# Performance work log

Hardware: AMD Instinct MI355X
Metric: run time of the kernel (lower is better)

## Reference

```python
import jax, jax.numpy as jnp
import numpy as np

B = 8192
DIMS = [1024, 1024, 1024, 1024]  # input, hidden0, hidden1, output
RANK = 64


def _apg_layer(x, Wm, bm, U, V, b, activate):
    # hyper-net (MLP_Layer with no hidden units == single Linear): generates rank*rank weights per sample
    w = (x @ Wm.T + bm).reshape(x.shape[0], RANK, RANK)   # [B, r, r]
    u = x @ U.T                                           # U_matrix: [B, r]
    # (u.unsqueeze(-1) * w).sum(-2) == per-sample matvec
    h = jnp.einsum('br,brs->bs', u, w)                    # [B, r]
    out = h @ V.T + b                                     # V_matrix + static bias: [B, out]
    return jax.nn.relu(out) if activate else out


def setup_inputs() -> dict:
    key = jax.random.key(0)
    ks = jax.random.split(key, 16)
    inp = {"x": jax.random.normal(ks[0], (B, DIMS[0]), dtype=jnp.float32)}
    ki = 1
    for l in range(3):
        din, dout = DIMS[l], DIMS[l + 1]
        inp[f"Wm{l}"] = jax.random.normal(ks[ki], (RANK * RANK, din), dtype=jnp.float32) * (1.0 / np.sqrt(din)); ki += 1
        inp[f"bm{l}"] = jnp.zeros((RANK * RANK,), dtype=jnp.float32)
        inp[f"U{l}"] = jax.random.normal(ks[ki], (RANK, din), dtype=jnp.float32) * (1.0 / np.sqrt(din)); ki += 1
        inp[f"V{l}"] = jax.random.normal(ks[ki], (dout, RANK), dtype=jnp.float32) * (1.0 / np.sqrt(RANK)); ki += 1
        inp[f"b{l}"] = jnp.zeros((dout,), dtype=jnp.float32)
    return inp


def reference(x, Wm0, bm0, U0, V0, b0, Wm1, bm1, U1, V1, b1, Wm2, bm2, U2, V2, b2):
    h = _apg_layer(x, Wm0, bm0, U0, V0, b0, activate=True)   # hidden layer 0 + ReLU
    h = _apg_layer(h, Wm1, bm1, U1, V1, b1, activate=True)   # hidden layer 1 + ReLU
    out = _apg_layer(h, Wm2, bm2, U2, V2, b2, activate=False)  # output layer, no activation
    return out
```

## Files before the change

kernel.cpp:

```cpp
#include <hip/hip_runtime.h>
#include <stdint.h>

typedef short bf16x8_t __attribute__((ext_vector_type(8)));
typedef short bf16x4_t __attribute__((ext_vector_type(4)));
typedef float f32x4_t __attribute__((ext_vector_type(4)));
typedef unsigned short u16x4_t __attribute__((ext_vector_type(4)));

#define DEV static __device__ __forceinline__

DEV float bf2f(unsigned short u) {
  union { unsigned int i; float f; } v; v.i = ((unsigned int)u) << 16; return v.f;
}
DEV unsigned short f2bf(float f) {
  union { float f; unsigned int i; } v; v.f = f;
  unsigned int x = v.i;
  unsigned int lsb = (x >> 16) & 1u;
  x += 0x7fffu + lsb;
  return (unsigned short)(x >> 16);
}

struct CvtTab {
  const float* src[10];
  unsigned short* dst[10];
  int bstart[10];
};

__global__ __launch_bounds__(256) void cvt_all_k(CvtTab t) {
  int bi = blockIdx.x;
  int seg = 0;
#pragma unroll
  for (int s = 1; s < 10; s++) seg += (bi >= t.bstart[s]) ? 1 : 0;
  int local = (bi - t.bstart[seg]) * 256 + threadIdx.x;
  const float* src = t.src[seg];
  unsigned short* dst = t.dst[seg];
  float4 v = ((const float4*)src)[local];
  u16x4_t o = { f2bf(v.x), f2bf(v.y), f2bf(v.z), f2bf(v.w) };
  *(u16x4_t*)&dst[local * 4] = o;
}

__global__ __launch_bounds__(256, 2) void u_splitk(
    const unsigned short* __restrict__ A,
    const unsigned short* __restrict__ Ub,
    float* __restrict__ part) {
  __shared__ unsigned short As[128 * 64];
  __shared__ unsigned short Us[64 * 64];

  const int tid = threadIdx.x;
  const int lane = tid & 63;
  const int w = tid >> 6;
  const int rowBase = blockIdx.y * 128;
  const int kBase = blockIdx.x * 256;

  const int rl = lane >> 3;
  const int kbs = lane & 7;
  const int kbg = kbs ^ rl;
  const int fr = lane & 15;
  const int quad = lane >> 4;

  f32x4_t acc[2][4];
#pragma unroll
  for (int i = 0; i < 2; i++)
#pragma unroll
    for (int j = 0; j < 4; j++) acc[i][j] = f32x4_t{0.f, 0.f, 0.f, 0.f};

  for (int kt = kBase; kt < kBase + 256; kt += 64) {
    __syncthreads();
#pragma unroll
    for (int jj = 0; jj < 4; ++jj) {
      int tr = w * 32 + jj * 8 + rl;
      const unsigned short* ga = A + (size_t)(rowBase + tr) * 1024 + kt + kbg * 8;
      __builtin_amdgcn_global_load_lds(
          (const __attribute__((address_space(1))) void*)ga,
          (__attribute__((address_space(3))) void*)&As[(w * 32 + jj * 8) * 64],
          16, 0, 0);
    }
#pragma unroll
    for (int jj = 0; jj < 2; ++jj) {
      int tr = w * 16 + jj * 8 + rl;
      const unsigned short* gu = Ub + (size_t)tr * 1024 + kt + kbg * 8;
      __builtin_amdgcn_global_load_lds(
          (const __attribute__((address_space(1))) void*)gu,
          (__attribute__((address_space(3))) void*)&Us[(w * 16 + jj * 8) * 64],
          16, 0, 0);
    }
    __syncthreads();

#pragma unroll
    for (int ks = 0; ks < 2; ++ks) {
      bf16x8_t a[2], b[4];
#pragma unroll
      for (int i = 0; i < 2; i++) {
        int m = w * 32 + i * 16 + fr;
        int slot = (ks * 4 + quad) ^ (m & 7);
        a[i] = *(const bf16x8_t*)&As[m * 64 + slot * 8];
      }
#pragma unroll
      for (int j = 0; j < 4; j++) {
        int n = j * 16 + fr;
        int slot = (ks * 4 + quad) ^ (n & 7);
        b[j] = *(const bf16x8_t*)&Us[n * 64 + slot * 8];
      }
#pragma unroll
      for (int i = 0; i < 2; i++)
#pragma unroll
        for (int j = 0; j < 4; j++)
          acc[i][j] = __builtin_amdgcn_mfma_f32_16x16x32_bf16(a[i], b[j],
                                                              acc[i][j], 0, 0, 0);
    }
  }

  float* pp = part + ((size_t)blockIdx.x * 8192 + rowBase) * 64;
#pragma unroll
  for (int i = 0; i < 2; i++)
#pragma unroll
    for (int j = 0; j < 4; j++)
#pragma unroll
      for (int r = 0; r < 4; r++) {
        int row = w * 32 + i * 16 + quad * 4 + r;
        pp[(size_t)row * 64 + j * 16 + fr] = acc[i][j][r];
      }
}

__global__ __launch_bounds__(256) void u_reduce_k(
    const float* __restrict__ part, unsigned short* __restrict__ ug) {
  int i = blockIdx.x * 256 + threadIdx.x;
  float4 s0 = ((const float4*)part)[i];
  float4 s1 = ((const float4*)part)[i + 131072];
  float4 s2 = ((const float4*)part)[i + 262144];
  float4 s3 = ((const float4*)part)[i + 393216];
  u16x4_t o = { f2bf(s0.x + s1.x + s2.x + s3.x),
                f2bf(s0.y + s1.y + s2.y + s3.y),
                f2bf(s0.z + s1.z + s2.z + s3.z),
                f2bf(s0.w + s1.w + s2.w + s3.w) };
  *(u16x4_t*)&ug[i * 4] = o;
}

template <int OUTF32, int RELU, int BIAS>
__global__ __launch_bounds__(256, 2) void gemm_bt(
    const unsigned short* __restrict__ A, const unsigned short* __restrict__ B,
    const float* __restrict__ bias, void* __restrict__ Cout,
    int M, int N, int K) {
  __shared__ unsigned short As[128 * 64];
  __shared__ unsigned short Bs[128 * 64];

  const int tid = threadIdx.x;
  const int lane = tid & 63;
  const int w = tid >> 6;
  const int wrow0 = (w & 1) * 64;
  const int wcol0 = (w >> 1) * 64;
  const int rowBase = blockIdx.y * 128;
  const int colBase = blockIdx.x * 128;

  const int rl = lane >> 3;
  const int kbs = lane & 7;
  const int kbg = kbs ^ rl;
  const int fr = lane & 15;
  const int quad = lane >> 4;

  f32x4_t acc[4][4];
#pragma unroll
  for (int i = 0; i < 4; i++)
#pragma unroll
    for (int j = 0; j < 4; j++) acc[i][j] = f32x4_t{0.f, 0.f, 0.f, 0.f};

  for (int kt = 0; kt < K; kt += 64) {
    __syncthreads();
#pragma unroll
    for (int jj = 0; jj < 4; ++jj) {
      int tr = w * 32 + jj * 8 + rl;
      const unsigned short* ga = A + (size_t)(rowBase + tr) * K + kt + kbg * 8;
      const unsigned short* gb = B + (size_t)(colBase + tr) * K + kt + kbg * 8;
      __builtin_amdgcn_global_load_lds(
          (const __attribute__((address_space(1))) void*)ga,
          (__attribute__((address_space(3))) void*)&As[(w * 32 + jj * 8) * 64],
          16, 0, 0);
      __builtin_amdgcn_global_load_lds(
          (const __attribute__((address_space(1))) void*)gb,
          (__attribute__((address_space(3))) void*)&Bs[(w * 32 + jj * 8) * 64],
          16, 0, 0);
    }
    __syncthreads();

#pragma unroll
    for (int ks = 0; ks < 2; ++ks) {
      bf16x8_t a[4], b[4];
#pragma unroll
      for (int i = 0; i < 4; i++) {
        int m = wrow0 + i * 16 + fr;
        int slot = (ks * 4 + quad) ^ (m & 7);
        a[i] = *(const bf16x8_t*)&As[m * 64 + slot * 8];
      }
#pragma unroll
      for (int j = 0; j < 4; j++) {
        int n = wcol0 + j * 16 + fr;
        int slot = (ks * 4 + quad) ^ (n & 7);
        b[j] = *(const bf16x8_t*)&Bs[n * 64 + slot * 8];
      }
#pragma unroll
      for (int i = 0; i < 4; i++)
#pragma unroll
        for (int j = 0; j < 4; j++)
          acc[i][j] = __builtin_amdgcn_mfma_f32_16x16x32_bf16(a[i], b[j],
                                                              acc[i][j], 0, 0, 0);
    }
  }

#pragma unroll
  for (int j = 0; j < 4; j++) {
    int col = colBase + wcol0 + j * 16 + fr;
    float bv = BIAS ? bias[col] : 0.0f;
#pragma unroll
    for (int i = 0; i < 4; i++) {
#pragma unroll
      for (int r = 0; r < 4; r++) {
        int row = rowBase + wrow0 + i * 16 + quad * 4 + r;
        float v = acc[i][j][r] + bv;
        if (RELU) v = v > 0.f ? v : 0.f;
        if (OUTF32)
          ((float*)Cout)[(size_t)row * N + col] = v;
        else
          ((unsigned short*)Cout)[(size_t)row * N + col] = f2bf(v);
      }
    }
  }
}

__global__ __launch_bounds__(256, 2) void gemm_fused(
    const unsigned short* __restrict__ A,
    const unsigned short* __restrict__ Wmb,
    const unsigned short* __restrict__ ug,
    const float* __restrict__ bm,
    unsigned short* __restrict__ h_out) {
  __shared__ unsigned short smem[16384];
  unsigned short* As = smem;
  unsigned short* Bs = smem + 8192;
  const int K = 1024;

  const int tid = threadIdx.x;
  const int lane = tid & 63;
  const int w = tid >> 6;
  const int wrow0 = (w & 1) * 64;
  const int wcol0 = (w >> 1) * 64;
  const int rowBase = blockIdx.y * 128;
  const int colBase = blockIdx.x * 128;

  const int rl = lane >> 3;
  const int kbs = lane & 7;
  const int kbg = kbs ^ rl;
  const int fr = lane & 15;
  const int quad = lane >> 4;

  f32x4_t acc[4][4];
#pragma unroll
  for (int i = 0; i < 4; i++)
#pragma unroll
    for (int j = 0; j < 4; j++) acc[i][j] = f32x4_t{0.f, 0.f, 0.f, 0.f};

  for (int kt = 0; kt < K; kt += 64) {
    __syncthreads();
#pragma unroll
    for (int jj = 0; jj < 4; ++jj) {
      int tr = w * 32 + jj * 8 + rl;
      int ct = colBase + tr;
      int pr = ((ct & 63) << 6) | (ct >> 6);
      const unsigned short* ga = A + (size_t)(rowBase + tr) * K + kt + kbg * 8;
      const unsigned short* gb = Wmb + (size_t)pr * K + kt + kbg * 8;
      __builtin_amdgcn_global_load_lds(
          (const __attribute__((address_space(1))) void*)ga,
          (__attribute__((address_space(3))) void*)&As[(w * 32 + jj * 8) * 64],
          16, 0, 0);
      __builtin_amdgcn_global_load_lds(
          (const __attribute__((address_space(1))) void*)gb,
          (__attribute__((address_space(3))) void*)&Bs[(w * 32 + jj * 8) * 64],
          16, 0, 0);
    }
    __syncthreads();

#pragma unroll
    for (int ks = 0; ks < 2; ++ks) {
      bf16x8_t a[4], b[4];
#pragma unroll
      for (int i = 0; i < 4; i++) {
        int m = wrow0 + i * 16 + fr;
        int slot = (ks * 4 + quad) ^ (m & 7);
        a[i] = *(const bf16x8_t*)&As[m * 64 + slot * 8];
      }
#pragma unroll
      for (int j = 0; j < 4; j++) {
        int n = wcol0 + j * 16 + fr;
        int slot = (ks * 4 + quad) ^ (n & 7);
        b[j] = *(const bf16x8_t*)&Bs[n * 64 + slot * 8];
      }
#pragma unroll
      for (int i = 0; i < 4; i++)
#pragma unroll
        for (int j = 0; j < 4; j++)
          acc[i][j] = __builtin_amdgcn_mfma_f32_16x16x32_bf16(a[i], b[j],
                                                              acc[i][j], 0, 0, 0);
    }
  }

  __syncthreads();

  {
    int row = tid >> 1;
    int c0 = (tid & 1) * 32;
    const unsigned short* up = ug + (size_t)(rowBase + row) * 64 + c0;
    bf16x8_t v0 = *(const bf16x8_t*)(up);
    bf16x8_t v1 = *(const bf16x8_t*)(up + 8);
    bf16x8_t v2 = *(const bf16x8_t*)(up + 16);
    bf16x8_t v3 = *(const bf16x8_t*)(up + 24);
#pragma unroll
    for (int m = 0; m < 8; m++) {
      smem[(c0 + m) * 136 + row] = (unsigned short)v0[m];
      smem[(c0 + 8 + m) * 136 + row] = (unsigned short)v1[m];
      smem[(c0 + 16 + m) * 136 + row] = (unsigned short)v2[m];
      smem[(c0 + 24 + m) * 136 + row] = (unsigned short)v3[m];
    }
  }
  __syncthreads();

  const int s = blockIdx.x * 2 + (w >> 1);
  float bmv[4];
#pragma unroll
  for (int j = 0; j < 4; j++) bmv[j] = bm[(j * 16 + fr) * 64 + s];

#pragma unroll
  for (int i = 0; i < 4; i++) {
    int row0 = wrow0 + i * 16 + quad * 4;
    bf16x4_t uv[4];
#pragma unroll
    for (int j = 0; j < 4; j++)
      uv[j] = *(const bf16x4_t*)&smem[(j * 16 + fr) * 136 + row0];
#pragma unroll
    for (int r = 0; r < 4; r++) {
      float p = 0.f;
#pragma unroll
      for (int j = 0; j < 4; j++)
        p += bf2f((unsigned short)uv[j][r]) * (acc[i][j][r] + bmv[j]);
      p += __shfl_xor(p, 1, 64);
      p += __shfl_xor(p, 2, 64);
      p += __shfl_xor(p, 4, 64);
      p += __shfl_xor(p, 8, 64);
      if (fr == 0)
        h_out[(size_t)(rowBase + row0 + r) * 64 + s] = f2bf(p);
    }
  }
}

__global__ __launch_bounds__(256, 2) void vu_fused(
    const unsigned short* __restrict__ h,
    const unsigned short* __restrict__ Vb,
    const float* __restrict__ bias,
    const unsigned short* __restrict__ Un,
    unsigned short* __restrict__ act,
    unsigned short* __restrict__ u_out) {
  __shared__ unsigned short tlds[4 * 16 * 72];
  __shared__ float upart[4 * 16 * 68];

  const int tid = threadIdx.x;
  const int lane = tid & 63;
  const int w = tid >> 6;
  const int fr = lane & 15;
  const int quad = lane >> 4;
  const int rowBase = blockIdx.x * 16;

  unsigned short* tl = &tlds[w * 16 * 72];

  bf16x8_t ah0 = *(const bf16x8_t*)&h[(size_t)(rowBase + fr) * 64 + quad * 8];
  bf16x8_t ah1 = *(const bf16x8_t*)&h[(size_t)(rowBase + fr) * 64 + 32 + quad * 8];

  f32x4_t uacc[4];
#pragma unroll
  for (int n = 0; n < 4; n++) uacc[n] = f32x4_t{0.f, 0.f, 0.f, 0.f};

  for (int it = 0; it < 4; ++it) {
    const int cb = w * 256 + it * 64;

    f32x4_t tacc[4];
#pragma unroll
    for (int nt = 0; nt < 4; nt++) {
      const unsigned short* vrow = Vb + (size_t)(cb + nt * 16 + fr) * 64;
      bf16x8_t b0 = *(const bf16x8_t*)&vrow[quad * 8];
      bf16x8_t b1 = *(const bf16x8_t*)&vrow[32 + quad * 8];
      f32x4_t z = {0.f, 0.f, 0.f, 0.f};
      z = __builtin_amdgcn_mfma_f32_16x16x32_bf16(ah0, b0, z, 0, 0, 0);
      tacc[nt] = __builtin_amdgcn_mfma_f32_16x16x32_bf16(ah1, b1, z, 0, 0, 0);
    }

#pragma unroll
    for (int nt = 0; nt < 4; nt++) {
      float bv = bias[cb + nt * 16 + fr];
#pragma unroll
      for (int r = 0; r < 4; r++) {
        float v = tacc[nt][r] + bv;
        v = v > 0.f ? v : 0.f;
        tl[(quad * 4 + r) * 72 + nt * 16 + fr] = f2bf(v);
      }
    }

    {
      int m2 = lane >> 2;
      int kc = (lane & 3) * 16;
      bf16x8_t t0 = *(const bf16x8_t*)&tl[m2 * 72 + kc];
      bf16x8_t t1 = *(const bf16x8_t*)&tl[m2 * 72 + kc + 8];
      unsigned short* ap = act + (size_t)(rowBase + m2) * 1024 + cb + kc;
      *(bf16x8_t*)ap = t0;
      *(bf16x8_t*)(ap + 8) = t1;
    }

#pragma unroll
    for (int ks = 0; ks < 2; ++ks) {
      bf16x8_t at = *(const bf16x8_t*)&tl[fr * 72 + ks * 32 + quad * 8];
#pragma unroll
      for (int n = 0; n < 4; n++) {
        bf16x8_t bu = *(const bf16x8_t*)&Un[(size_t)(n * 16 + fr) * 1024 + cb +
                                            ks * 32 + quad * 8];
        uacc[n] = __builtin_amdgcn_mfma_f32_16x16x32_bf16(at, bu, uacc[n], 0, 0, 0);
      }
    }
  }

  {
    float* up = &upart[w * 16 * 68];
#pragma unroll
    for (int n = 0; n < 4; n++)
#pragma unroll
      for (int r = 0; r < 4; r++)
        up[(quad * 4 + r) * 68 + n * 16 + fr] = uacc[n][r];
  }
  __syncthreads();
  {
    int m = tid >> 4;
    int c0 = (tid & 15) * 4;
    f32x4_t s = {0.f, 0.f, 0.f, 0.f};
#pragma unroll
    for (int wv = 0; wv < 4; wv++)
      s += *(const f32x4_t*)&upart[wv * 16 * 68 + m * 68 + c0];
    u16x4_t o = { f2bf(s[0]), f2bf(s[1]), f2bf(s[2]), f2bf(s[3]) };
    *(u16x4_t*)&u_out[(size_t)(rowBase + m) * 64 + c0] = o;
  }
}

extern "C" void kernel_launch(void* const* d_in, const int* in_sizes, int n_in,
                              void* d_out, int out_size, void* d_ws,
                              size_t ws_size, hipStream_t stream) {
  const float* x = (const float*)d_in[0];
  const float* Wm[3] = {(const float*)d_in[1], (const float*)d_in[6], (const float*)d_in[11]};
  const float* bm[3] = {(const float*)d_in[2], (const float*)d_in[7], (const float*)d_in[12]};
  const float* U[3]  = {(const float*)d_in[3], (const float*)d_in[8], (const float*)d_in[13]};
  const float* V[3]  = {(const float*)d_in[4], (const float*)d_in[9], (const float*)d_in[14]};
  const float* bs[3] = {(const float*)d_in[5], (const float*)d_in[10], (const float*)d_in[15]};

  char* p = (char*)d_ws;
  unsigned short* xb = (unsigned short*)p;  p += 8192UL * 1024 * 2;
  unsigned short* act = (unsigned short*)p; p += 8192UL * 1024 * 2;
  unsigned short* Wmb[3];
  for (int l = 0; l < 3; l++) { Wmb[l] = (unsigned short*)p; p += 4096UL * 1024 * 2; }
  unsigned short* Ub[3];
  for (int l = 0; l < 3; l++) { Ub[l] = (unsigned short*)p; p += 64UL * 1024 * 2; }
  unsigned short* Vb[3];
  for (int l = 0; l < 3; l++) { Vb[l] = (unsigned short*)p; p += 1024UL * 64 * 2; }
  unsigned short* hb = (unsigned short*)p;  p += 8192UL * 64 * 2;
  unsigned short* ug = (unsigned short*)p;  p += 8192UL * 64 * 2;
  float* ug_part = (float*)p;               p += 4UL * 8192 * 64 * 4;

  CvtTab t;
  t.src[0] = x;  t.dst[0] = xb;
  for (int l = 0; l < 3; l++) { t.src[1 + l] = Wm[l]; t.dst[1 + l] = Wmb[l]; }
  for (int l = 0; l < 3; l++) { t.src[4 + l] = U[l];  t.dst[4 + l] = Ub[l]; }
  for (int l = 0; l < 3; l++) { t.src[7 + l] = V[l];  t.dst[7 + l] = Vb[l]; }
  int bs_tab[10] = {8192, 4096, 4096, 4096, 64, 64, 64, 64, 64, 64};
  int acc_b = 0;
  for (int s = 0; s < 10; s++) { t.bstart[s] = acc_b; acc_b += bs_tab[s]; }
  cvt_all_k<<<acc_b, 256, 0, stream>>>(t);

  u_splitk<<<dim3(4, 64), 256, 0, stream>>>(xb, Ub[0], ug_part);
  u_reduce_k<<<512, 256, 0, stream>>>(ug_part, ug);

  const unsigned short* cur = xb;
  for (int l = 0; l < 3; l++) {
    gemm_fused<<<dim3(32, 64), 256, 0, stream>>>(cur, Wmb[l], ug, bm[l], hb);
    if (l < 2) {
      vu_fused<<<512, 256, 0, stream>>>(hb, Vb[l], bs[l], Ub[l + 1], act, ug);
      cur = act;
    } else {
      gemm_bt<1, 0, 1><<<dim3(8, 64), 256, 0, stream>>>(
          hb, Vb[2], bs[2], d_out, 8192, 1024, 64);
    }
  }
}
```

Measured before the change: 420.9 us.

## Merge all phases into one persistent cooperative kernel with grid syncs

Replaces the chain of separate launches (convert, U split-K, reduce, three hyper-GEMMs, VU fused, final GEMM) with a single cooperative persistent kernel. Phases are separated by grid-wide syncs, and hyper-GEMM tiles are handed out through atomic counters. The U0 split-K now uses 8 slices of 128 instead of 4 of 256. This removes launch gaps and tail effects between kernels, at the cost of grid-sync overhead, a fixed grid size and possibly lower occupancy for the persistent blocks. A fallback path keeps the multi-kernel launches.

```diff
diff --git a/kernel.cpp b/kernel.cpp
--- a/kernel.cpp
+++ b/kernel.cpp
@@ -1,5 +1,8 @@
 #include <hip/hip_runtime.h>
+#include <hip/hip_cooperative_groups.h>
 #include <stdint.h>
+
+namespace cg = cooperative_groups;
 
 typedef short bf16x8_t __attribute__((ext_vector_type(8)));
 typedef short bf16x4_t __attribute__((ext_vector_type(4)));
@@ -19,41 +22,50 @@
   return (unsigned short)(x >> 16);
 }
 
-struct CvtTab {
-  const float* src[10];
-  unsigned short* dst[10];
-  int bstart[10];
+struct MegaArgs {
+  const float* fsrc[10];
+  unsigned short* fdst[10];
+  const float* bm[3];
+  const float* bb[3];
+  unsigned short* xb;
+  unsigned short* act;
+  unsigned short* Wmb[3];
+  unsigned short* Ub[3];
+  unsigned short* Vb[3];
+  unsigned short* hb;
+  unsigned short* ug;
+  float* ug_part;
+  float* out;
+  int* counters;
 };
 
-__global__ __launch_bounds__(256) void cvt_all_k(CvtTab t) {
-  int bi = blockIdx.x;
-  int seg = 0;
-#pragma unroll
-  for (int s = 1; s < 10; s++) seg += (bi >= t.bstart[s]) ? 1 : 0;
-  int local = (bi - t.bstart[seg]) * 256 + threadIdx.x;
-  const float* src = t.src[seg];
-  unsigned short* dst = t.dst[seg];
-  float4 v = ((const float4*)src)[local];
-  u16x4_t o = { f2bf(v.x), f2bf(v.y), f2bf(v.z), f2bf(v.w) };
-  *(u16x4_t*)&dst[local * 4] = o;
-}
-
-__global__ __launch_bounds__(256, 2) void u_splitk(
-    const unsigned short* __restrict__ A,
-    const unsigned short* __restrict__ Ub,
-    float* __restrict__ part) {
-  __shared__ unsigned short As[128 * 64];
-  __shared__ unsigned short Us[64 * 64];
-
-  const int tid = threadIdx.x;
+DEV void phase_cvt(const MegaArgs& A, int bid, int tid, int NB) {
+  const int bstart[11] = {0, 8192, 12288, 16384, 20480, 20544, 20608,
+                          20672, 20736, 20800, 20864};
+  for (int vb = bid; vb < 20864; vb += NB) {
+    int seg = 0;
+#pragma unroll
+    for (int s = 1; s < 10; s++) seg += (vb >= bstart[s]) ? 1 : 0;
+    int local = (vb - bstart[seg]) * 256 + tid;
+    float4 v = ((const float4*)A.fsrc[seg])[local];
+    u16x4_t o = { f2bf(v.x), f2bf(v.y), f2bf(v.z), f2bf(v.w) };
+    *(u16x4_t*)&A.fdst[seg][local * 4] = o;
+  }
+}
+
+DEV void u0_splitk_vb(const unsigned short* __restrict__ Acur,
+                      const unsigned short* __restrict__ Ub,
+                      float* __restrict__ part,
+                      unsigned short* smem, int vb, int tid) {
+  unsigned short* As = smem;
+  unsigned short* Us = smem + 8192;
   const int lane = tid & 63;
   const int w = tid >> 6;
-  const int rowBase = blockIdx.y * 128;
-  const int kBase = blockIdx.x * 256;
-
+  const int ks = vb >> 6;
+  const int rowBase = (vb & 63) * 128;
+  const int kBase = ks * 128;
   const int rl = lane >> 3;
-  const int kbs = lane & 7;
-  const int kbg = kbs ^ rl;
+  const int kbg = (lane & 7) ^ rl;
   const int fr = lane & 15;
   const int quad = lane >> 4;
 
@@ -63,12 +75,12 @@
 #pragma unroll
     for (int j = 0; j < 4; j++) acc[i][j] = f32x4_t{0.f, 0.f, 0.f, 0.f};
 
-  for (int kt = kBase; kt < kBase + 256; kt += 64) {
+  for (int kt = kBase; kt < kBase + 128; kt += 64) {
     __syncthreads();
 #pragma unroll
     for (int jj = 0; jj < 4; ++jj) {
       int tr = w * 32 + jj * 8 + rl;
-      const unsigned short* ga = A + (size_t)(rowBase + tr) * 1024 + kt + kbg * 8;
+      const unsigned short* ga = Acur + (size_t)(rowBase + tr) * 1024 + kt + kbg * 8;
       __builtin_amdgcn_global_load_lds(
           (const __attribute__((address_space(1))) void*)ga,
           (__attribute__((address_space(3))) void*)&As[(w * 32 + jj * 8) * 64],
@@ -86,18 +98,18 @@
     __syncthreads();
 
 #pragma unroll
-    for (int ks = 0; ks < 2; ++ks) {
+    for (int ksi = 0; ksi < 2; ++ksi) {
       bf16x8_t a[2], b[4];
 #pragma unroll
       for (int i = 0; i < 2; i++) {
         int m = w * 32 + i * 16 + fr;
-        int slot = (ks * 4 + quad) ^ (m & 7);
+        int slot = (ksi * 4 + quad) ^ (m & 7);
         a[i] = *(const bf16x8_t*)&As[m * 64 + slot * 8];
       }
 #pragma unroll
       for (int j = 0; j < 4; j++) {
         int n = j * 16 + fr;
-        int slot = (ks * 4 + quad) ^ (n & 7);
+        int slot = (ksi * 4 + quad) ^ (n & 7);
         b[j] = *(const bf16x8_t*)&Us[n * 64 + slot * 8];
       }
 #pragma unroll
@@ -109,7 +121,7 @@
     }
   }
 
-  float* pp = part + ((size_t)blockIdx.x * 8192 + rowBase) * 64;
+  float* pp = part + ((size_t)ks * 8192 + rowBase) * 64;
 #pragma unroll
   for (int i = 0; i < 2; i++)
 #pragma unroll
@@ -121,41 +133,41 @@
       }
 }
 
-__global__ __launch_bounds__(256) void u_reduce_k(
-    const float* __restrict__ part, unsigned short* __restrict__ ug) {
-  int i = blockIdx.x * 256 + threadIdx.x;
-  float4 s0 = ((const float4*)part)[i];
-  float4 s1 = ((const float4*)part)[i + 131072];
-  float4 s2 = ((const float4*)part)[i + 262144];
-  float4 s3 = ((const float4*)part)[i + 393216];
-  u16x4_t o = { f2bf(s0.x + s1.x + s2.x + s3.x),
-                f2bf(s0.y + s1.y + s2.y + s3.y),
-                f2bf(s0.z + s1.z + s2.z + s3.z),
-                f2bf(s0.w + s1.w + s2.w + s3.w) };
-  *(u16x4_t*)&ug[i * 4] = o;
-}
-
-template <int OUTF32, int RELU, int BIAS>
-__global__ __launch_bounds__(256, 2) void gemm_bt(
-    const unsigned short* __restrict__ A, const unsigned short* __restrict__ B,
-    const float* __restrict__ bias, void* __restrict__ Cout,
-    int M, int N, int K) {
-  __shared__ unsigned short As[128 * 64];
-  __shared__ unsigned short Bs[128 * 64];
-
-  const int tid = threadIdx.x;
+DEV void phase_u0_reduce(const float* __restrict__ part,
+                         unsigned short* __restrict__ ug,
+                         int bid, int tid, int NB) {
+  for (int vb = bid; vb < 512; vb += NB) {
+    int i = vb * 256 + tid;
+    f32x4_t s = {0.f, 0.f, 0.f, 0.f};
+#pragma unroll
+    for (int sl = 0; sl < 8; sl++)
+      s += *(const f32x4_t*)&part[(i + sl * 131072) * 4];
+    u16x4_t o = { f2bf(s[0]), f2bf(s[1]), f2bf(s[2]), f2bf(s[3]) };
+    *(u16x4_t*)&ug[i * 4] = o;
+  }
+}
+
+DEV void hyper_tile(const unsigned short* __restrict__ Acur,
+                    const unsigned short* __restrict__ Wmb,
+                    const unsigned short* __restrict__ ug,
+                    const float* __restrict__ bm,
+                    unsigned short* __restrict__ h_out,
+                    unsigned short* smem, int vb, int tid) {
   const int lane = tid & 63;
   const int w = tid >> 6;
   const int wrow0 = (w & 1) * 64;
   const int wcol0 = (w >> 1) * 64;
-  const int rowBase = blockIdx.y * 128;
-  const int colBase = blockIdx.x * 128;
-
   const int rl = lane >> 3;
-  const int kbs = lane & 7;
-  const int kbg = kbs ^ rl;
+  const int kbg = (lane & 7) ^ rl;
   const int fr = lane & 15;
   const int quad = lane >> 4;
+  unsigned short* As = smem;
+  unsigned short* Bs = smem + 8192;
+
+  const int bx = vb >> 6;
+  const int by = vb & 63;
+  const int rowBase = by * 128;
+  const int colBase = bx * 128;
 
   f32x4_t acc[4][4];
 #pragma unroll
@@ -163,13 +175,15 @@
 #pragma unroll
     for (int j = 0; j < 4; j++) acc[i][j] = f32x4_t{0.f, 0.f, 0.f, 0.f};
 
-  for (int kt = 0; kt < K; kt += 64) {
+  for (int kt = 0; kt < 1024; kt += 64) {
     __syncthreads();
 #pragma unroll
     for (int jj = 0; jj < 4; ++jj) {
       int tr = w * 32 + jj * 8 + rl;
-      const unsigned short* ga = A + (size_t)(rowBase + tr) * K + kt + kbg * 8;
-      const unsigned short* gb = B + (size_t)(colBase + tr) * K + kt + kbg * 8;
+      int ct = colBase + tr;
+      int pr = ((ct & 63) << 6) | (ct >> 6);
+      const unsigned short* ga = Acur + (size_t)(rowBase + tr) * 1024 + kt + kbg * 8;
+      const unsigned short* gb = Wmb + (size_t)pr * 1024 + kt + kbg * 8;
       __builtin_amdgcn_global_load_lds(
           (const __attribute__((address_space(1))) void*)ga,
           (__attribute__((address_space(3))) void*)&As[(w * 32 + jj * 8) * 64],
@@ -205,103 +219,7 @@
     }
   }
 
-#pragma unroll
-  for (int j = 0; j < 4; j++) {
-    int col = colBase + wcol0 + j * 16 + fr;
-    float bv = BIAS ? bias[col] : 0.0f;
-#pragma unroll
-    for (int i = 0; i < 4; i++) {
-#pragma unroll
-      for (int r = 0; r < 4; r++) {
-        int row = rowBase + wrow0 + i * 16 + quad * 4 + r;
-        float v = acc[i][j][r] + bv;
-        if (RELU) v = v > 0.f ? v : 0.f;
-        if (OUTF32)
-          ((float*)Cout)[(size_t)row * N + col] = v;
-        else
-          ((unsigned short*)Cout)[(size_t)row * N + col] = f2bf(v);
-      }
-    }
-  }
-}
-
-__global__ __launch_bounds__(256, 2) void gemm_fused(
-    const unsigned short* __restrict__ A,
-    const unsigned short* __restrict__ Wmb,
-    const unsigned short* __restrict__ ug,
-    const float* __restrict__ bm,
-    unsigned short* __restrict__ h_out) {
-  __shared__ unsigned short smem[16384];
-  unsigned short* As = smem;
-  unsigned short* Bs = smem + 8192;
-  const int K = 1024;
-
-  const int tid = threadIdx.x;
-  const int lane = tid & 63;
-  const int w = tid >> 6;
-  const int wrow0 = (w & 1) * 64;
-  const int wcol0 = (w >> 1) * 64;
-  const int rowBase = blockIdx.y * 128;
-  const int colBase = blockIdx.x * 128;
-
-  const int rl = lane >> 3;
-  const int kbs = lane & 7;
-  const int kbg = kbs ^ rl;
-  const int fr = lane & 15;
-  const int quad = lane >> 4;
-
-  f32x4_t acc[4][4];
-#pragma unroll
-  for (int i = 0; i < 4; i++)
-#pragma unroll
-    for (int j = 0; j < 4; j++) acc[i][j] = f32x4_t{0.f, 0.f, 0.f, 0.f};
-
-  for (int kt = 0; kt < K; kt += 64) {
-    __syncthreads();
-#pragma unroll
-    for (int jj = 0; jj < 4; ++jj) {
-      int tr = w * 32 + jj * 8 + rl;
-      int ct = colBase + tr;
-      int pr = ((ct & 63) << 6) | (ct >> 6);
-      const unsigned short* ga = A + (size_t)(rowBase + tr) * K + kt + kbg * 8;
-      const unsigned short* gb = Wmb + (size_t)pr * K + kt + kbg * 8;
-      __builtin_amdgcn_global_load_lds(
-          (const __attribute__((address_space(1))) void*)ga,
-          (__attribute__((address_space(3))) void*)&As[(w * 32 + jj * 8) * 64],
-          16, 0, 0);
-      __builtin_amdgcn_global_load_lds(
-          (const __attribute__((address_space(1))) void*)gb,
-          (__attribute__((address_space(3))) void*)&Bs[(w * 32 + jj * 8) * 64],
-          16, 0, 0);
-    }
-    __syncthreads();
-
-#pragma unroll
-    for (int ks = 0; ks < 2; ++ks) {
-      bf16x8_t a[4], b[4];
-#pragma unroll
-      for (int i = 0; i < 4; i++) {
-        int m = wrow0 + i * 16 + fr;
-        int slot = (ks * 4 + quad) ^ (m & 7);
-        a[i] = *(const bf16x8_t*)&As[m * 64 + slot * 8];
-      }
-#pragma unroll
-      for (int j = 0; j < 4; j++) {
-        int n = wcol0 + j * 16 + fr;
-        int slot = (ks * 4 + quad) ^ (n & 7);
-        b[j] = *(const bf16x8_t*)&Bs[n * 64 + slot * 8];
-      }
-#pragma unroll
-      for (int i = 0; i < 4; i++)
-#pragma unroll
-        for (int j = 0; j < 4; j++)
-          acc[i][j] = __builtin_amdgcn_mfma_f32_16x16x32_bf16(a[i], b[j],
-                                                              acc[i][j], 0, 0, 0);
-    }
-  }
-
   __syncthreads();
-
   {
     int row = tid >> 1;
     int c0 = (tid & 1) * 32;
@@ -320,7 +238,7 @@
   }
   __syncthreads();
 
-  const int s = blockIdx.x * 2 + (w >> 1);
+  const int s = bx * 2 + (w >> 1);
   float bmv[4];
 #pragma unroll
   for (int j = 0; j < 4; j++) bmv[j] = bm[(j * 16 + fr) * 64 + s];
@@ -348,22 +266,23 @@
   }
 }
 
-__global__ __launch_bounds__(256, 2) void vu_fused(
-    const unsigned short* __restrict__ h,
-    const unsigned short* __restrict__ Vb,
-    const float* __restrict__ bias,
-    const unsigned short* __restrict__ Un,
-    unsigned short* __restrict__ act,
-    unsigned short* __restrict__ u_out) {
-  __shared__ unsigned short tlds[4 * 16 * 72];
-  __shared__ float upart[4 * 16 * 68];
-
-  const int tid = threadIdx.x;
+DEV void vu_vb(const unsigned short* __restrict__ h,
+               const unsigned short* __restrict__ Vb,
+               const float* __restrict__ bias,
+               const unsigned short* __restrict__ Un,
+               unsigned short* __restrict__ act,
+               unsigned short* __restrict__ u_out,
+               unsigned char* smem_raw, int vb, int tid) {
+  unsigned short* tlds = (unsigned short*)smem_raw;
+  float* upart = (float*)(smem_raw + 9216);
+
   const int lane = tid & 63;
   const int w = tid >> 6;
   const int fr = lane & 15;
   const int quad = lane >> 4;
-  const int rowBase = blockIdx.x * 16;
+  const int rowBase = vb * 16;
+
+  __syncthreads();
 
   unsigned short* tl = &tlds[w * 16 * 72];
 
@@ -440,6 +359,164 @@
     u16x4_t o = { f2bf(s[0]), f2bf(s[1]), f2bf(s[2]), f2bf(s[3]) };
     *(u16x4_t*)&u_out[(size_t)(rowBase + m) * 64 + c0] = o;
   }
+}
+
+DEV void final_vb(const unsigned short* __restrict__ Ah,
+                  const unsigned short* __restrict__ Bv,
+                  const float* __restrict__ bias,
+                  float* __restrict__ Cout,
+                  unsigned short* smem, int vb, int tid) {
+  unsigned short* As = smem;
+  unsigned short* Bs = smem + 8192;
+  const int lane = tid & 63;
+  const int w = tid >> 6;
+  const int wrow0 = (w & 1) * 64;
+  const int wcol0 = (w >> 1) * 64;
+  const int rowBase = (vb & 63) * 128;
+  const int colBase = (vb >> 6) * 128;
+  const int rl = lane >> 3;
+  const int kbg = (lane & 7) ^ rl;
+  const int fr = lane & 15;
+  const int quad = lane >> 4;
+
+  f32x4_t acc[4][4];
+#pragma unroll
+  for (int i = 0; i < 4; i++)
+#pragma unroll
+    for (int j = 0; j < 4; j++) acc[i][j] = f32x4_t{0.f, 0.f, 0.f, 0.f};
+
+  __syncthreads();
+#pragma unroll
+  for (int jj = 0; jj < 4; ++jj) {
+    int tr = w * 32 + jj * 8 + rl;
+    const unsigned short* ga = Ah + (size_t)(rowBase + tr) * 64 + kbg * 8;
+    const unsigned short* gb = Bv + (size_t)(colBase + tr) * 64 + kbg * 8;
+    __builtin_amdgcn_global_load_lds(
+        (const __attribute__((address_space(1))) void*)ga,
+        (__attribute__((address_space(3))) void*)&As[(w * 32 + jj * 8) * 64],
+        16, 0, 0);
+    __builtin_amdgcn_global_load_lds(
+        (const __attribute__((address_space(1))) void*)gb,
+        (__attribute__((address_space(3))) void*)&Bs[(w * 32 + jj * 8) * 64],
+        16, 0, 0);
+  }
+  __syncthreads();
+
+#pragma unroll
+  for (int ks = 0; ks < 2; ++ks) {
+    bf16x8_t a[4], b[4];
+#pragma unroll
+    for (int i = 0; i < 4; i++) {
+      int m = wrow0 + i * 16 + fr;
+      int slot = (ks * 4 + quad) ^ (m & 7);
+      a[i] = *(const bf16x8_t*)&As[m * 64 + slot * 8];
+    }
+#pragma unroll
+    for (int j = 0; j < 4; j++) {
+      int n = wcol0 + j * 16 + fr;
+      int slot = (ks * 4 + quad) ^ (n & 7);
+      b[j] = *(const bf16x8_t*)&Bs[n * 64 + slot * 8];
+    }
+#pragma unroll
+    for (int i = 0; i < 4; i++)
+#pragma unroll
+      for (int j = 0; j < 4; j++)
+        acc[i][j] = __builtin_amdgcn_mfma_f32_16x16x32_bf16(a[i], b[j],
+                                                            acc[i][j], 0, 0, 0);
+  }
+
+#pragma unroll
+  for (int j = 0; j < 4; j++) {
+    int col = colBase + wcol0 + j * 16 + fr;
+    float bv = bias[col];
+#pragma unroll
+    for (int i = 0; i < 4; i++) {
+#pragma unroll
+      for (int r = 0; r < 4; r++) {
+        int row = rowBase + wrow0 + i * 16 + quad * 4 + r;
+        Cout[(size_t)row * 1024 + col] = acc[i][j][r] + bv;
+      }
+    }
+  }
+}
+
+__global__ __launch_bounds__(256, 2) void mega_k(MegaArgs A) {
+  __shared__ alignas(16) unsigned char smem_raw[32768];
+  __shared__ int s_tile;
+  unsigned short* smem = (unsigned short*)smem_raw;
+  cg::grid_group g = cg::this_grid();
+  const int bid = blockIdx.x;
+  const int tid = threadIdx.x;
+  const int NB = gridDim.x;
+
+  if (bid == 0 && tid < 8) A.counters[tid] = 0;
+
+  phase_cvt(A, bid, tid, NB);
+  g.sync();
+
+  for (int vb = bid; vb < 512; vb += NB)
+    u0_splitk_vb(A.xb, A.Ub[0], A.ug_part, smem, vb, tid);
+  g.sync();
+
+  phase_u0_reduce(A.ug_part, A.ug, bid, tid, NB);
+  g.sync();
+
+  const unsigned short* cur = A.xb;
+#pragma unroll 1
+  for (int l = 0; l < 3; l++) {
+    for (;;) {
+      if (tid == 0) s_tile = atomicAdd(&A.counters[l], 1);
+      __syncthreads();
+      int vb = s_tile;
+      __syncthreads();
+      if (vb >= 2048) break;
+      hyper_tile(cur, A.Wmb[l], A.ug, A.bm[l], A.hb, smem, vb, tid);
+    }
+    g.sync();
+
+    if (l < 2) {
+      for (int vb = bid; vb < 512; vb += NB)
+        vu_vb(A.hb, A.Vb[l], A.bb[l], A.Ub[l + 1], A.act, A.ug, smem_raw, vb, tid);
+      g.sync();
+      cur = A.act;
+    } else {
+      for (int vb = bid; vb < 512; vb += NB)
+        final_vb(A.hb, A.Vb[2], A.bb[2], A.out, smem, vb, tid);
+    }
+  }
+}
+
+__global__ __launch_bounds__(256) void k_cvt(MegaArgs A) {
+  phase_cvt(A, blockIdx.x, threadIdx.x, gridDim.x);
+}
+__global__ __launch_bounds__(256, 2) void k_u0_splitk(MegaArgs A) {
+  __shared__ unsigned short smem[12288];
+  for (int vb = blockIdx.x; vb < 512; vb += gridDim.x)
+    u0_splitk_vb(A.xb, A.Ub[0], A.ug_part, smem, vb, threadIdx.x);
+}
+__global__ __launch_bounds__(256) void k_u0_reduce(MegaArgs A) {
+  phase_u0_reduce(A.ug_part, A.ug, blockIdx.x, threadIdx.x, gridDim.x);
+}
+__global__ __launch_bounds__(256, 2) void k_hyper(
+    const unsigned short* __restrict__ Acur,
+    const unsigned short* __restrict__ Wmb,
+    const unsigned short* __restrict__ ug, const float* __restrict__ bm,
+    unsigned short* __restrict__ hb) {
+  __shared__ unsigned short smem[16384];
+  hyper_tile(Acur, Wmb, ug, bm, hb, smem, blockIdx.x, threadIdx.x);
+}
+__global__ __launch_bounds__(256, 2) void k_vu(
+    const unsigned short* __restrict__ h, const unsigned short* __restrict__ Vb,
+    const float* __restrict__ bias, const unsigned short* __restrict__ Un,
+    unsigned short* __restrict__ act, unsigned short* __restrict__ u_out) {
+  __shared__ alignas(16) unsigned char smem_raw[28672];
+  vu_vb(h, Vb, bias, Un, act, u_out, smem_raw, blockIdx.x, threadIdx.x);
+}
+__global__ __launch_bounds__(256, 2) void k_final(
+    const unsigned short* __restrict__ Ah, const unsigned short* __restrict__ Bv,
+    const float* __restrict__ bias, float* __restrict__ Cout) {
+  __shared__ unsigned short smem[12288];
+  final_vb(Ah, Bv, bias, Cout, smem, blockIdx.x, threadIdx.x);
 }
 
 extern "C" void kernel_launch(void* const* d_in, const int* in_sizes, int n_in,
@@ -463,30 +540,55 @@
   for (int l = 0; l < 3; l++) { Vb[l] = (unsigned short*)p; p += 1024UL * 64 * 2; }
   unsigned short* hb = (unsigned short*)p;  p += 8192UL * 64 * 2;
   unsigned short* ug = (unsigned short*)p;  p += 8192UL * 64 * 2;
-  float* ug_part = (float*)p;               p += 4UL * 8192 * 64 * 4;
-
-  CvtTab t;
-  t.src[0] = x;  t.dst[0] = xb;
-  for (int l = 0; l < 3; l++) { t.src[1 + l] = Wm[l]; t.dst[1 + l] = Wmb[l]; }
-  for (int l = 0; l < 3; l++) { t.src[4 + l] = U[l];  t.dst[4 + l] = Ub[l]; }
-  for (int l = 0; l < 3; l++) { t.src[7 + l] = V[l];  t.dst[7 + l] = Vb[l]; }
-  int bs_tab[10] = {8192, 4096, 4096, 4096, 64, 64, 64, 64, 64, 64};
-  int acc_b = 0;
-  for (int s = 0; s < 10; s++) { t.bstart[s] = acc_b; acc_b += bs_tab[s]; }
-  cvt_all_k<<<acc_b, 256, 0, stream>>>(t);
-
-  u_splitk<<<dim3(4, 64), 256, 0, stream>>>(xb, Ub[0], ug_part);
-  u_reduce_k<<<512, 256, 0, stream>>>(ug_part, ug);
-
-  const unsigned short* cur = xb;
+  float* ug_part = (float*)p;               p += 8UL * 8192 * 64 * 4;
+  int* counters = (int*)p;                  p += 64;
+
+  MegaArgs A;
+  A.fsrc[0] = x;  A.fdst[0] = xb;
+  for (int l = 0; l < 3; l++) { A.fsrc[1 + l] = Wm[l]; A.fdst[1 + l] = Wmb[l]; }
+  for (int l = 0; l < 3; l++) { A.fsrc[4 + l] = U[l];  A.fdst[4 + l] = Ub[l]; }
+  for (int l = 0; l < 3; l++) { A.fsrc[7 + l] = V[l];  A.fdst[7 + l] = Vb[l]; }
   for (int l = 0; l < 3; l++) {
-    gemm_fused<<<dim3(32, 64), 256, 0, stream>>>(cur, Wmb[l], ug, bm[l], hb);
-    if (l < 2) {
-      vu_fused<<<512, 256, 0, stream>>>(hb, Vb[l], bs[l], Ub[l + 1], act, ug);
-      cur = act;
-    } else {
-      gemm_bt<1, 0, 1><<<dim3(8, 64), 256, 0, stream>>>(
-          hb, Vb[2], bs[2], d_out, 8192, 1024, 64);
-    }
-  }
-}
+    A.bm[l] = bm[l]; A.bb[l] = bs[l];
+    A.Wmb[l] = Wmb[l]; A.Ub[l] = Ub[l]; A.Vb[l] = Vb[l];
+  }
+  A.xb = xb; A.act = act; A.hb = hb; A.ug = ug;
+  A.ug_part = ug_part; A.out = (float*)d_out; A.counters = counters;
+
+  int maxPerCU = 0;
+  (void)hipOccupancyMaxActiveBlocksPerMultiprocessor(&maxPerCU, mega_k, 256, 0);
+  int numCU = 256;
+  {
+    int dev = 0;
+    (void)hipGetDevice(&dev);
+    (void)hipDeviceGetAttribute(&numCU, hipDeviceAttributeMultiprocessorCount,
+                                dev);
+  }
+  bool coop_done = false;
+  if (maxPerCU >= 1) {
+    long cap = (long)maxPerCU * numCU;
+    int NB = (int)(cap < 768 ? cap : 768);
+    if (NB >= 256) {
+      void* kargs[] = {(void*)&A};
+      hipError_t e = hipLaunchCooperativeKernel(mega_k, dim3(NB), dim3(256),
+                                                kargs, 0u, stream);
+      coop_done = (e == hipSuccess);
+    }
+  }
+
+  if (!coop_done) {
+    k_cvt<<<20864, 256, 0, stream>>>(A);
+    k_u0_splitk<<<512, 256, 0, stream>>>(A);
+    k_u0_reduce<<<512, 256, 0, stream>>>(A);
+    const unsigned short* cur = xb;
+    for (int l = 0; l < 3; l++) {
+      k_hyper<<<2048, 256, 0, stream>>>(cur, Wmb[l], ug, bm[l], hb);
+      if (l < 2) {
+        k_vu<<<512, 256, 0, stream>>>(hb, Vb[l], bs[l], Ub[l + 1], act, ug);
+        cur = act;
+      } else {
+        k_final<<<512, 256, 0, stream>>>(hb, Vb[2], bs[2], (float*)d_out);
+      }
+    }
+  }
+}
```

Result: slower. 990.6 us (+135.4%).

## Overlap next-layer weight conversion with hyper-net GEMM via extra grid blocks

Applied to the files above, without the earlier changes.

The single upfront fp32→bf16 conversion of all weights is split so that only x, Wm0 and U0 are converted first. Later layers' weights are converted by extra blocks appended to the preceding hyper GEMM launch, so the conversion overlaps with the compute-bound GEMM. The hyper GEMM now uses a flattened 1D grid, and the final K=64 GEMM is specialised with its loop removed. The cost is extra blocks competing for CUs during the GEMM tail.

```diff
diff --git a/kernel.cpp b/kernel.cpp
--- a/kernel.cpp
+++ b/kernel.cpp
@@ -19,23 +19,22 @@
   return (unsigned short)(x >> 16);
 }
 
-struct CvtTab {
-  const float* src[10];
-  unsigned short* dst[10];
-  int bstart[10];
+struct CvtSeg {
+  const float* src[3];
+  unsigned short* dst[3];
+  int bstart[4];
 };
 
-__global__ __launch_bounds__(256) void cvt_all_k(CvtTab t) {
-  int bi = blockIdx.x;
-  int seg = 0;
-#pragma unroll
-  for (int s = 1; s < 10; s++) seg += (bi >= t.bstart[s]) ? 1 : 0;
-  int local = (bi - t.bstart[seg]) * 256 + threadIdx.x;
-  const float* src = t.src[seg];
-  unsigned short* dst = t.dst[seg];
-  float4 v = ((const float4*)src)[local];
+DEV void cvt_block(const CvtSeg& cs, int vb, int tid) {
+  int seg = (vb >= cs.bstart[1] ? 1 : 0) + (vb >= cs.bstart[2] ? 1 : 0);
+  int local = (vb - cs.bstart[seg]) * 256 + tid;
+  float4 v = ((const float4*)cs.src[seg])[local];
   u16x4_t o = { f2bf(v.x), f2bf(v.y), f2bf(v.z), f2bf(v.w) };
-  *(u16x4_t*)&dst[local * 4] = o;
+  *(u16x4_t*)&cs.dst[seg][local * 4] = o;
+}
+
+__global__ __launch_bounds__(256) void k_cvt(CvtSeg cs) {
+  cvt_block(cs, blockIdx.x, threadIdx.x);
 }
 
 __global__ __launch_bounds__(256, 2) void u_splitk(
@@ -52,8 +51,7 @@
   const int kBase = blockIdx.x * 256;
 
   const int rl = lane >> 3;
-  const int kbs = lane & 7;
-  const int kbg = kbs ^ rl;
+  const int kbg = (lane & 7) ^ rl;
   const int fr = lane & 15;
   const int quad = lane >> 4;
 
@@ -135,118 +133,36 @@
   *(u16x4_t*)&ug[i * 4] = o;
 }
 
-template <int OUTF32, int RELU, int BIAS>
-__global__ __launch_bounds__(256, 2) void gemm_bt(
-    const unsigned short* __restrict__ A, const unsigned short* __restrict__ B,
-    const float* __restrict__ bias, void* __restrict__ Cout,
-    int M, int N, int K) {
-  __shared__ unsigned short As[128 * 64];
-  __shared__ unsigned short Bs[128 * 64];
+__global__ __launch_bounds__(256, 2) void k_hyper(
+    const unsigned short* __restrict__ A,
+    const unsigned short* __restrict__ Wmb,
+    const unsigned short* __restrict__ ug,
+    const float* __restrict__ bm,
+    unsigned short* __restrict__ h_out,
+    CvtSeg cs) {
+  __shared__ unsigned short smem[16384];
+
+  if (blockIdx.x >= 2048) {
+    cvt_block(cs, blockIdx.x - 2048, threadIdx.x);
+    return;
+  }
+
+  unsigned short* As = smem;
+  unsigned short* Bs = smem + 8192;
+  const int K = 1024;
 
   const int tid = threadIdx.x;
   const int lane = tid & 63;
   const int w = tid >> 6;
   const int wrow0 = (w & 1) * 64;
   const int wcol0 = (w >> 1) * 64;
-  const int rowBase = blockIdx.y * 128;
-  const int colBase = blockIdx.x * 128;
+  const int bx = blockIdx.x & 31;
+  const int by = blockIdx.x >> 5;
+  const int rowBase = by * 128;
+  const int colBase = bx * 128;
 
   const int rl = lane >> 3;
-  const int kbs = lane & 7;
-  const int kbg = kbs ^ rl;
-  const int fr = lane & 15;
-  const int quad = lane >> 4;
-
-  f32x4_t acc[4][4];
-#pragma unroll
-  for (int i = 0; i < 4; i++)
-#pragma unroll
-    for (int j = 0; j < 4; j++) acc[i][j] = f32x4_t{0.f, 0.f, 0.f, 0.f};
-
-  for (int kt = 0; kt < K; kt += 64) {
-    __syncthreads();
-#pragma unroll
-    for (int jj = 0; jj < 4; ++jj) {
-      int tr = w * 32 + jj * 8 + rl;
-      const unsigned short* ga = A + (size_t)(rowBase + tr) * K + kt + kbg * 8;
-      const unsigned short* gb = B + (size_t)(colBase + tr) * K + kt + kbg * 8;
-      __builtin_amdgcn_global_load_lds(
-          (const __attribute__((address_space(1))) void*)ga,
-          (__attribute__((address_space(3))) void*)&As[(w * 32 + jj * 8) * 64],
-          16, 0, 0);
-      __builtin_amdgcn_global_load_lds(
-          (const __attribute__((address_space(1))) void*)gb,
-          (__attribute__((address_space(3))) void*)&Bs[(w * 32 + jj * 8) * 64],
-          16, 0, 0);
-    }
-    __syncthreads();
-
-#pragma unroll
-    for (int ks = 0; ks < 2; ++ks) {
-      bf16x8_t a[4], b[4];
-#pragma unroll
-      for (int i = 0; i < 4; i++) {
-        int m = wrow0 + i * 16 + fr;
-        int slot = (ks * 4 + quad) ^ (m & 7);
-        a[i] = *(const bf16x8_t*)&As[m * 64 + slot * 8];
-      }
-#pragma unroll
-      for (int j = 0; j < 4; j++) {
-        int n = wcol0 + j * 16 + fr;
-        int slot = (ks * 4 + quad) ^ (n & 7);
-        b[j] = *(const bf16x8_t*)&Bs[n * 64 + slot * 8];
-      }
-#pragma unroll
-      for (int i = 0; i < 4; i++)
-#pragma unroll
-        for (int j = 0; j < 4; j++)
-          acc[i][j] = __builtin_amdgcn_mfma_f32_16x16x32_bf16(a[i], b[j],
-                                                              acc[i][j], 0, 0, 0);
-    }
-  }
-
-#pragma unroll
-  for (int j = 0; j < 4; j++) {
-    int col = colBase + wcol0 + j * 16 + fr;
-    float bv = BIAS ? bias[col] : 0.0f;
-#pragma unroll
-    for (int i = 0; i < 4; i++) {
-#pragma unroll
-      for (int r = 0; r < 4; r++) {
-        int row = rowBase + wrow0 + i * 16 + quad * 4 + r;
-        float v = acc[i][j][r] + bv;
-        if (RELU) v = v > 0.f ? v : 0.f;
-        if (OUTF32)
-          ((float*)Cout)[(size_t)row * N + col] = v;
-        else
-          ((unsigned short*)Cout)[(size_t)row * N + col] = f2bf(v);
-      }
-    }
-  }
-}
-
-__global__ __launch_bounds__(256, 2) void gemm_fused(
-    const unsigned short* __restrict__ A,
-    const unsigned short* __restrict__ Wmb,
-    const unsigned short* __restrict__ ug,
-    const float* __restrict__ bm,
-    unsigned short* __restrict__ h_out) {
-  __shared__ unsigned short smem[16384];
-  unsigned short* As = smem;
-  unsigned short* Bs = smem + 8192;
-  const int K = 1024;
-
-  const int tid = threadIdx.x;
-  const int lane = tid & 63;
-  const int w = tid >> 6;
-  const int wrow0 = (w & 1) * 64;
-  const int wcol0 = (w >> 1) * 64;
-  const int rowBase = blockIdx.y * 128;
-  const int colBase = blockIdx.x * 128;
-
-  const int rl = lane >> 3;
-  const int kbs = lane & 7;
-  const int kbg = kbs ^ rl;
+  const int kbg = (lane & 7) ^ rl;
   const int fr = lane & 15;
   const int quad = lane >> 4;
 
@@ -320,7 +236,7 @@
   }
   __syncthreads();
 
-  const int s = blockIdx.x * 2 + (w >> 1);
+  const int s = bx * 2 + (w >> 1);
   float bmv[4];
 #pragma unroll
   for (int j = 0; j < 4; j++) bmv[j] = bm[(j * 16 + fr) * 64 + s];
@@ -439,6 +355,86 @@
       s += *(const f32x4_t*)&upart[wv * 16 * 68 + m * 68 + c0];
     u16x4_t o = { f2bf(s[0]), f2bf(s[1]), f2bf(s[2]), f2bf(s[3]) };
     *(u16x4_t*)&u_out[(size_t)(rowBase + m) * 64 + c0] = o;
+  }
+}
+
+__global__ __launch_bounds__(256, 2) void k_final(
+    const unsigned short* __restrict__ A, const unsigned short* __restrict__ B,
+    const float* __restrict__ bias, float* __restrict__ Cout) {
+  __shared__ unsigned short As[128 * 64];
+  __shared__ unsigned short Bs[128 * 64];
+
+  const int tid = threadIdx.x;
+  const int lane = tid & 63;
+  const int w = tid >> 6;
+  const int wrow0 = (w & 1) * 64;
+  const int wcol0 = (w >> 1) * 64;
+  const int rowBase = blockIdx.y * 128;
+  const int colBase = blockIdx.x * 128;
+
+  const int rl = lane >> 3;
+  const int kbg = (lane & 7) ^ rl;
+  const int fr = lane & 15;
+  const int quad = lane >> 4;
+
+  f32x4_t acc[4][4];
+#pragma unroll
+  for (int i = 0; i < 4; i++)
+#pragma unroll
+    for (int j = 0; j < 4; j++) acc[i][j] = f32x4_t{0.f, 0.f, 0.f, 0.f};
+
+  __syncthreads();
+#pragma unroll
+  for (int jj = 0; jj < 4; ++jj) {
+    int tr = w * 32 + jj * 8 + rl;
+    const unsigned short* ga = A + (size_t)(rowBase + tr) * 64 + kbg * 8;
+    const unsigned short* gb = B + (size_t)(colBase + tr) * 64 + kbg * 8;
+    __builtin_amdgcn_global_load_lds(
+        (const __attribute__((address_space(1))) void*)ga,
+        (__attribute__((address_space(3))) void*)&As[(w * 32 + jj * 8) * 64],
+        16, 0, 0);
+    __builtin_amdgcn_global_load_lds(
+        (const __attribute__((address_space(1))) void*)gb,
+        (__attribute__((address_space(3))) void*)&Bs[(w * 32 + jj * 8) * 64],
+        16, 0, 0);
+  }
+  __syncthreads();
+
+#pragma unroll
+  for (int ks = 0; ks < 2; ++ks) {
+    bf16x8_t a[4], b[4];
+#pragma unroll
+    for (int i = 0; i < 4; i++) {
+      int m = wrow0 + i * 16 + fr;
+      int slot = (ks * 4 + quad) ^ (m & 7);
+      a[i] = *(const bf16x8_t*)&As[m * 64 + slot * 8];
+    }
+#pragma unroll
+    for (int j = 0; j < 4; j++) {
+      int n = wcol0 + j * 16 + fr;
+      int slot = (ks * 4 + quad) ^ (n & 7);
+      b[j] = *(const bf16x8_t*)&Bs[n * 64 + slot * 8];
+    }
+#pragma unroll
+    for (int i = 0; i < 4; i++)
+#pragma unroll
+      for (int j = 0; j < 4; j++)
+        acc[i][j] = __builtin_amdgcn_mfma_f32_16x16x32_bf16(a[i], b[j],
+                                                            acc[i][j], 0, 0, 0);
+  }
+
+#pragma unroll
+  for (int j = 0; j < 4; j++) {
+    int col = colBase + wcol0 + j * 16 + fr;
+    float bv = bias[col];
+#pragma unroll
+    for (int i = 0; i < 4; i++) {
+#pragma unroll
+      for (int r = 0; r < 4; r++) {
+        int row = rowBase + wrow0 + i * 16 + quad * 4 + r;
+        Cout[(size_t)row * 1024 + col] = acc[i][j][r] + bv;
+      }
+    }
   }
 }
 
@@ -465,28 +461,40 @@
   unsigned short* ug = (unsigned short*)p;  p += 8192UL * 64 * 2;
   float* ug_part = (float*)p;               p += 4UL * 8192 * 64 * 4;
 
-  CvtTab t;
-  t.src[0] = x;  t.dst[0] = xb;
-  for (int l = 0; l < 3; l++) { t.src[1 + l] = Wm[l]; t.dst[1 + l] = Wmb[l]; }
-  for (int l = 0; l < 3; l++) { t.src[4 + l] = U[l];  t.dst[4 + l] = Ub[l]; }
-  for (int l = 0; l < 3; l++) { t.src[7 + l] = V[l];  t.dst[7 + l] = Vb[l]; }
-  int bs_tab[10] = {8192, 4096, 4096, 4096, 64, 64, 64, 64, 64, 64};
-  int acc_b = 0;
-  for (int s = 0; s < 10; s++) { t.bstart[s] = acc_b; acc_b += bs_tab[s]; }
-  cvt_all_k<<<acc_b, 256, 0, stream>>>(t);
+  CvtSeg c0;
+  c0.src[0] = x;     c0.dst[0] = xb;
+  c0.src[1] = Wm[0]; c0.dst[1] = Wmb[0];
+  c0.src[2] = U[0];  c0.dst[2] = Ub[0];
+  c0.bstart[0] = 0; c0.bstart[1] = 8192; c0.bstart[2] = 12288; c0.bstart[3] = 12352;
+  k_cvt<<<12352, 256, 0, stream>>>(c0);
 
   u_splitk<<<dim3(4, 64), 256, 0, stream>>>(xb, Ub[0], ug_part);
   u_reduce_k<<<512, 256, 0, stream>>>(ug_part, ug);
 
+  CvtSeg ch[3];
+  ch[0].src[0] = Wm[1]; ch[0].dst[0] = Wmb[1];
+  ch[0].src[1] = U[1];  ch[0].dst[1] = Ub[1];
+  ch[0].src[2] = V[0];  ch[0].dst[2] = Vb[0];
+  ch[0].bstart[0] = 0; ch[0].bstart[1] = 4096; ch[0].bstart[2] = 4160; ch[0].bstart[3] = 4224;
+  ch[1].src[0] = Wm[2]; ch[1].dst[0] = Wmb[2];
+  ch[1].src[1] = U[2];  ch[1].dst[1] = Ub[2];
+  ch[1].src[2] = V[1];  ch[1].dst[2] = Vb[1];
+  ch[1].bstart[0] = 0; ch[1].bstart[1] = 4096; ch[1].bstart[2] = 4160; ch[1].bstart[3] = 4224;
+  ch[2].src[0] = V[2]; ch[2].dst[0] = Vb[2];
+  ch[2].src[1] = V[2]; ch[2].dst[1] = Vb[2];
+  ch[2].src[2] = V[2]; ch[2].dst[2] = Vb[2];
+  ch[2].bstart[0] = 0; ch[2].bstart[1] = 64; ch[2].bstart[2] = 64; ch[2].bstart[3] = 64;
+
+  const int hyperGrid[3] = {2048 + 4224, 2048 + 4224, 2048 + 64};
+
   const unsigned short* cur = xb;
   for (int l = 0; l < 3; l++) {
-    gemm_fused<<<dim3(32, 64), 256, 0, stream>>>(cur, Wmb[l], ug, bm[l], hb);
+    k_hyper<<<hyperGrid[l], 256, 0, stream>>>(cur, Wmb[l], ug, bm[l], hb, ch[l]);
     if (l < 2) {
       vu_fused<<<512, 256, 0, stream>>>(hb, Vb[l], bs[l], Ub[l + 1], act, ug);
       cur = act;
     } else {
-      gemm_bt<1, 0, 1><<<dim3(8, 64), 256, 0, stream>>>(
-          hb, Vb[2], bs[2], d_out, 8192, 1024, 64);
-    }
-  }
-}
+      k_final<<<dim3(8, 64), 256, 0, stream>>>(hb, Vb[2], bs[2], (float*)d_out);
+    }
+  }
+}
```

Result: no change. 415.8 us (-1.2%).
